# Kernel optimization log

Measured on AMD Instinct MI355X. Metric: run time of the kernel, lower is better.

## Reference

```python
import jax, jax.numpy as jnp
import numpy as np
import math

HEADS = 32
GROUPS = 8
HEAD_DIM = 64
HIDDEN = 2048
B, S = 2, 2048


def _rope(x, freqs_cis):
    # x: (..., S, head_dim); freqs_cis: (S, head_dim) -> interleaved cos/sin pattern
    x_even = x[..., ::2]
    x_odd = x[..., 1::2]
    cos = freqs_cis[..., ::2]
    sin = freqs_cis[..., 1::2]
    r_even = x_even * cos - x_odd * sin
    r_odd = x_even * sin + x_odd * cos
    return jnp.stack([r_even, r_odd], axis=-1).reshape(x.shape)


def setup_inputs() -> dict:
    key = jax.random.key(0)
    ks = jax.random.split(key, 12)
    scale = 1.0 / math.sqrt(HIDDEN)
    x = jax.random.normal(ks[0], (B, S, HIDDEN), dtype=jnp.float32)
    freqs_cis = jax.random.uniform(ks[1], (S, HEAD_DIM), dtype=jnp.float32)
    causal = jnp.tril(jnp.ones((S, S), dtype=bool))
    mask = jnp.where(causal, 0.0, -1e9).astype(jnp.float32)
    kv_dims = HEAD_DIM * GROUPS
    wq = jax.random.normal(ks[2], (HIDDEN, HIDDEN), jnp.float32) * scale
    bq = jnp.zeros((HIDDEN,), jnp.float32)
    wk = jax.random.normal(ks[3], (kv_dims, HIDDEN), jnp.float32) * scale
    bk = jnp.zeros((kv_dims,), jnp.float32)
    wv = jax.random.normal(ks[4], (kv_dims, HIDDEN), jnp.float32) * scale
    bv = jnp.zeros((kv_dims,), jnp.float32)
    wo = jax.random.normal(ks[5], (HIDDEN, HIDDEN), jnp.float32) * scale
    bo = jnp.zeros((HIDDEN,), jnp.float32)
    return dict(x=x, freqs_cis=freqs_cis, mask=mask, wq=wq, bq=bq,
                wk=wk, bk=bk, wv=wv, bv=bv, wo=wo, bo=bo)


def reference(x, freqs_cis, mask, wq, bq, wk, bk, wv, bv, wo, bo):
    b, s, h = x.shape
    rep = HEADS // GROUPS
    q = x @ wq.T + bq                      # (B,S,H)
    k = x @ wk.T + bk                      # (B,S,G*hd)
    v = x @ wv.T + bv
    q = q.reshape(b, s, HEADS, HEAD_DIM).transpose(0, 2, 1, 3)   # (B,Hh,S,hd)
    k = k.reshape(b, s, GROUPS, HEAD_DIM).transpose(0, 2, 1, 3)  # (B,G,S,hd)
    v = v.reshape(b, s, GROUPS, HEAD_DIM).transpose(0, 2, 1, 3)
    q = _rope(q, freqs_cis)
    k = _rope(k, freqs_cis)
    # GQA: group q heads instead of materially repeating K/V
    qg = q.reshape(b, GROUPS, rep, s, HEAD_DIM)
    scores = jnp.einsum('bgrsd,bgtd->bgrst', qg, k) / math.sqrt(HEAD_DIM)
    scores = scores + mask                 # broadcast (S,S)
    attn = jax.nn.softmax(scores, axis=-1)
    out = jnp.einsum('bgrst,bgtd->bgrsd', attn, v)
    out = out.reshape(b, HEADS, s, HEAD_DIM).transpose(0, 2, 1, 3).reshape(b, s, h)
    return out @ wo.T + bo
```

## Files before the change

### kernel.cpp

```cpp
#include <hip/hip_runtime.h>

#define S_LEN 2048
#define HID   2048
#define NQH   32
#define NKV   8
#define HD    64

#define BM 128
#define BN 128
#define BK 32

typedef __bf16 bf16x8 __attribute__((ext_vector_type(8)));
typedef __bf16 bf16x4 __attribute__((ext_vector_type(4)));
typedef float  f32x4  __attribute__((ext_vector_type(4)));

#define MFMA16(a, b, c) __builtin_amdgcn_mfma_f32_16x16x32_bf16(a, b, c, 0, 0, 0)

__device__ __forceinline__ void async_copy16(const void* g, void* l) {
  __builtin_amdgcn_global_load_lds(
      (const __attribute__((address_space(1))) unsigned int*)g,
      (__attribute__((address_space(3))) unsigned int*)l, 16, 0, 0);
}

__global__ void cast_all_k(const float* __restrict__ x,  const float* __restrict__ wq,
                           const float* __restrict__ wk, const float* __restrict__ wv,
                           const float* __restrict__ wo,
                           __bf16* __restrict__ xb,  __bf16* __restrict__ wqb,
                           __bf16* __restrict__ wkb, __bf16* __restrict__ wvb,
                           __bf16* __restrict__ wob) {
  int bid = blockIdx.x;
  const float* in; __bf16* out; int base;
  if (bid < 8192)       { in = x;  out = xb;  base = bid; }
  else if (bid < 12288) { in = wq; out = wqb; base = bid - 8192; }
  else if (bid < 13312) { in = wk; out = wkb; base = bid - 12288; }
  else if (bid < 14336) { in = wv; out = wvb; base = bid - 13312; }
  else                  { in = wo; out = wob; base = bid - 14336; }
  int i = (base * 256 + threadIdx.x) * 4;
  float4 v = *(const float4*)(in + i);
  bf16x4 o;
  o[0] = (__bf16)v.x; o[1] = (__bf16)v.y; o[2] = (__bf16)v.z; o[3] = (__bf16)v.w;
  *(bf16x4*)(out + i) = o;
}

__device__ __forceinline__ void gemm_pipe(const __bf16* __restrict__ A,
                                          const __bf16* __restrict__ B,
                                          int m0, int n0, int K,
                                          __bf16 (&As)[2][BM][BK],
                                          __bf16 (&Bs)[2][BN][BK],
                                          f32x4 (&acc)[4][4]) {
  const int tid = threadIdx.x, wave = tid >> 6, lane = tid & 63;
  const int l15 = lane & 15, quad = lane >> 4;
  const int wr = wave >> 1, wc = wave & 1;

  const int srow   = tid >> 2;
  const int schunk = (tid & 3) ^ ((tid >> 3) & 3);
  const __bf16* ga = A + (size_t)(m0 + srow) * K + schunk * 8;
  const __bf16* gb = B + (size_t)(n0 + srow) * K + schunk * 8;

  const int co = (quad ^ ((l15 >> 1) & 3)) * 8;

  const int NT = K / BK;

#define STAGE(st, kt) do {                                              \
    async_copy16(ga + (kt),                  &As[st][wave * 16][0]);    \
    async_copy16(ga + (kt) + (size_t)64 * K, &As[st][64 + wave * 16][0]); \
    async_copy16(gb + (kt),                  &Bs[st][wave * 16][0]);    \
    async_copy16(gb + (kt) + (size_t)64 * K, &Bs[st][64 + wave * 16][0]); \
  } while (0)

  STAGE(0, 0);
  asm volatile("s_waitcnt vmcnt(0)" ::: "memory");
  __builtin_amdgcn_s_barrier();
  asm volatile("" ::: "memory");

  int s = 0;
#pragma unroll 2
  for (int t = 0; t < NT; t++) {
    if (t + 1 < NT) STAGE(s ^ 1, (t + 1) * BK);

    const __bf16* a0 = &As[s][wr * 64][0];
    const __bf16* b0 = &Bs[s][wc * 64][0];
    bf16x8 af[4], bfr[4];
#pragma unroll
    for (int mt = 0; mt < 4; mt++)
      af[mt] = *(const bf16x8*)(a0 + (mt * 16 + l15) * BK + co);
#pragma unroll
    for (int nt = 0; nt < 4; nt++)
      bfr[nt] = *(const bf16x8*)(b0 + (nt * 16 + l15) * BK + co);

    __builtin_amdgcn_s_setprio(1);
#pragma unroll
    for (int mt = 0; mt < 4; mt++)
#pragma unroll
      for (int nt = 0; nt < 4; nt++)
        acc[mt][nt] = MFMA16(af[mt], bfr[nt], acc[mt][nt]);
    __builtin_amdgcn_s_setprio(0);

    asm volatile("s_waitcnt vmcnt(0) lgkmcnt(0)" ::: "memory");
    __builtin_amdgcn_s_barrier();
    asm volatile("" ::: "memory");
    s ^= 1;
  }
#undef STAGE
}

__global__ __launch_bounds__(256, 4) void gemm_qkv_k(const __bf16* __restrict__ xb,
    const __bf16* __restrict__ wqb, const __bf16* __restrict__ wkb, const __bf16* __restrict__ wvb,
    const float* __restrict__ bq, const float* __restrict__ bk, const float* __restrict__ bv,
    const float* __restrict__ fr,
    __bf16* __restrict__ Qb, __bf16* __restrict__ Kb, __bf16* __restrict__ Vt) {
  __shared__ __align__(16) __bf16 As[2][BM][BK];
  __shared__ __align__(16) __bf16 Bs[2][BN][BK];
  const int by = blockIdx.y;
  const int m0 = blockIdx.x * BM;
  const __bf16* B; const float* bias; int n0;
  int mode;
  if (by < 16)      { B = wqb; bias = bq; n0 = by * 128;        mode = 0; }
  else if (by < 20) { B = wkb; bias = bk; n0 = (by - 16) * 128; mode = 1; }
  else              { B = wvb; bias = bv; n0 = (by - 20) * 128; mode = 2; }

  f32x4 acc[4][4] = {};
  gemm_pipe(xb, B, m0, n0, HID, As, Bs, acc);

  const int tid = threadIdx.x, wave = tid >> 6, lane = tid & 63;
  const int l15 = lane & 15, quad = lane >> 4;
  const int wr = wave >> 1, wc = wave & 1;

  if (mode == 2) {
#pragma unroll
    for (int nt = 0; nt < 4; nt++) {
      int col = n0 + wc * 64 + nt * 16 + l15;
      int g = col >> 6, d = col & 63;
      float bv2 = bias[col];
#pragma unroll
      for (int mt = 0; mt < 4; mt++) {
        int row = m0 + wr * 64 + mt * 16 + quad * 4;
        int b = row >> 11, sI = row & 2047;
        bf16x4 o;
#pragma unroll
        for (int r = 0; r < 4; r++) o[r] = (__bf16)(acc[mt][nt][r] + bv2);
        *(bf16x4*)(Vt + (((size_t)(b * NKV + g) * HD + d)) * S_LEN + sI) = o;
      }
    }
  } else if (mode == 0) {
#pragma unroll
    for (int nt = 0; nt < 4; nt++) {
      int col = n0 + wc * 64 + nt * 16 + l15;
      float bv2 = bias[col];
#pragma unroll
      for (int mt = 0; mt < 4; mt++) {
        int row = m0 + wr * 64 + mt * 16 + quad * 4;
#pragma unroll
        for (int r = 0; r < 4; r++)
          Qb[(size_t)(row + r) * HID + col] = (__bf16)(acc[mt][nt][r] + bv2);
      }
    }
  } else {
    const int dpar = l15 & 1;
#pragma unroll
    for (int nt = 0; nt < 4; nt++) {
      int col = n0 + wc * 64 + nt * 16 + l15;
      int d = col & 63;
      float bv2 = bias[col];
#pragma unroll
      for (int mt = 0; mt < 4; mt++) {
        int row = m0 + wr * 64 + mt * 16 + quad * 4;
        int sI = row & 2047;
#pragma unroll
        for (int r = 0; r < 4; r++) {
          float v = acc[mt][nt][r] + bv2;
          float p = __shfl_xor(v, 1, 64);
          float f = fr[(size_t)(sI + r) * HD + d];
          float fp = __shfl_xor(f, 1, 64);
          float o = dpar ? (p * f + v * fp) : (v * f - p * fp);
          Kb[(size_t)(row + r) * 512 + col] = (__bf16)o;
        }
      }
    }
  }
}

__global__ __launch_bounds__(256, 4) void gemm_out_k(const __bf16* __restrict__ A,
    const __bf16* __restrict__ Bw, const float* __restrict__ bias, float* __restrict__ C) {
  __shared__ __align__(16) __bf16 As[2][BM][BK];
  __shared__ __align__(16) __bf16 Bs[2][BN][BK];
  const int m0 = blockIdx.x * BM, n0 = blockIdx.y * BN;
  f32x4 acc[4][4] = {};
  gemm_pipe(A, Bw, m0, n0, HID, As, Bs, acc);
  const int tid = threadIdx.x, wave = tid >> 6, lane = tid & 63;
  const int l15 = lane & 15, quad = lane >> 4;
  const int wr = wave >> 1, wc = wave & 1;
#pragma unroll
  for (int nt = 0; nt < 4; nt++) {
    int col = n0 + wc * 64 + nt * 16 + l15;
    float bv = bias[col];
#pragma unroll
    for (int mt = 0; mt < 4; mt++) {
      int row = m0 + wr * 64 + mt * 16 + quad * 4;
#pragma unroll
      for (int r = 0; r < 4; r++)
        C[(size_t)(row + r) * HID + col] = acc[mt][nt][r] + bv;
    }
  }
}

__device__ __forceinline__ void rope8(bf16x8& q, const float* f, float sc) {
  float4 fa = *(const float4*)f;
  float4 fb = *(const float4*)(f + 4);
  float e, o;
  e = (float)q[0]; o = (float)q[1];
  q[0] = (__bf16)((e * fa.x - o * fa.y) * sc);
  q[1] = (__bf16)((e * fa.y + o * fa.x) * sc);
  e = (float)q[2]; o = (float)q[3];
  q[2] = (__bf16)((e * fa.z - o * fa.w) * sc);
  q[3] = (__bf16)((e * fa.w + o * fa.z) * sc);
  e = (float)q[4]; o = (float)q[5];
  q[4] = (__bf16)((e * fb.x - o * fb.y) * sc);
  q[5] = (__bf16)((e * fb.y + o * fb.x) * sc);
  e = (float)q[6]; o = (float)q[7];
  q[6] = (__bf16)((e * fb.z - o * fb.w) * sc);
  q[7] = (__bf16)((e * fb.w + o * fb.z) * sc);
}

__global__ __launch_bounds__(256, 4) void flash_k(const __bf16* __restrict__ Q,
                                                  const __bf16* __restrict__ K,
                                                  const __bf16* __restrict__ Vt,
                                                  const float* __restrict__ fr,
                                                  __bf16* __restrict__ O) {
  __shared__ __align__(64) __bf16 Ksm[64][64];
  __shared__ __align__(64) __bf16 Vsm[64][64];
  __shared__ __align__(64) __bf16 Psm[4][16][64];
  const int tid = threadIdx.x;
  const int wave = tid >> 6, lane = tid & 63;
  const int l15 = lane & 15, quad = lane >> 4;
  const int x7 = l15 & 7, l15h = l15 >> 3;
  const int bh = blockIdx.x;
  const int b = bh >> 5, h = bh & 31, g = h >> 2;

  const int srow = tid >> 2, sc = (tid & 3) * 16;
  const int r7 = srow & 7;
  const int w0 = (((sc >> 3))     ^ r7) * 8;
  const int w1 = (((sc >> 3) + 1) ^ r7) * 8;

  char* kbp = (char*)&Ksm[0][0];
  char* vbp = (char*)&Vsm[0][0];
  char* pbp = (char*)&Psm[0][0][0];
  int kr[2], pr[2], pw[4];
#pragma unroll
  for (int ks = 0; ks < 2; ks++) {
    kr[ks] = l15 * 128 + (((ks * 4 + quad) ^ x7) * 16);
    pr[ks] = wave * 2048 + kr[ks];
  }
#pragma unroll
  for (int nt = 0; nt < 4; nt++)
    pw[nt] = wave * 2048 + quad * 512 + x7 * 2 + (((2 * nt + l15h) ^ ((quad & 1) * 4)) * 16);

  bf16x8 ones;
#pragma unroll
  for (int j = 0; j < 8; j++) ones[j] = (__bf16)1.0f;

  const __bf16* kbase = K + ((size_t)b * S_LEN + srow) * (NKV * HD) + g * HD + sc;
  const __bf16* vbase = Vt + (((size_t)b * NKV + g) * HD + srow) * S_LEN + sc;
  const float QSC = 0.125f * 1.44269504f;

#pragma unroll 1
  for (int half = 0; half < 2; half++) {
    const int qt = half ? (31 - (int)blockIdx.y) : (int)blockIdx.y;
    const int wq0 = qt * 64 + wave * 16;

    const __bf16* qp = Q + ((size_t)(b * S_LEN + wq0 + l15)) * HID + h * HD + quad * 8;
    bf16x8 qf0 = *(const bf16x8*)qp;
    bf16x8 qf1 = *(const bf16x8*)(qp + 32);
    const float* fq = fr + (size_t)(wq0 + l15) * HD + quad * 8;
    rope8(qf0, fq, QSC);
    rope8(qf1, fq + 32, QSC);

    f32x4 acc[4] = {};
    f32x4 accs = {};

    const __bf16* kp = kbase;
    const __bf16* vp = vbase;
    uint4 k0 = *(const uint4*)kp, k1 = *(const uint4*)(kp + 8);
    uint4 v0 = *(const uint4*)vp, v1 = *(const uint4*)(vp + 8);

    for (int t = 0; t <= qt; t++) {
      const int kv0 = t * 64;
      __syncthreads();
      *(uint4*)&Ksm[srow][w0] = k0;
      *(uint4*)&Ksm[srow][w1] = k1;
      *(uint4*)&Vsm[srow][w0] = v0;
      *(uint4*)&Vsm[srow][w1] = v1;
      if (t < qt) {
        kp += 64 * NKV * HD;  vp += 64;
        k0 = *(const uint4*)kp; k1 = *(const uint4*)(kp + 8);
        v0 = *(const uint4*)vp; v1 = *(const uint4*)(vp + 8);
      }
      __syncthreads();

      if (kv0 > wq0 + 15) continue;

      bf16x8 kf[2][4];
#pragma unroll
      for (int ks = 0; ks < 2; ks++)
#pragma unroll
        for (int nt = 0; nt < 4; nt++)
          kf[ks][nt] = *(const bf16x8*)(kbp + (kr[ks] + nt * 2048));

      f32x4 sacc[4] = {};
#pragma unroll
      for (int nt = 0; nt < 4; nt++) {
        sacc[nt] = MFMA16(qf0, kf[0][nt], sacc[nt]);
        sacc[nt] = MFMA16(qf1, kf[1][nt], sacc[nt]);
      }
      const bool domask = (kv0 + 63 > wq0);
#pragma unroll
      for (int nt = 0; nt < 4; nt++) {
        int kv = kv0 + nt * 16 + l15;
        int qr = wq0 + quad * 4;
#pragma unroll
        for (int r = 0; r < 4; r++) {
          float p = __builtin_exp2f(sacc[nt][r]);
          if (domask && kv > qr + r) p = 0.f;
          *(__bf16*)(pbp + ((pw[nt] ^ (r << 4)) + r * 128)) = (__bf16)p;
        }
      }

#pragma unroll
      for (int ks = 0; ks < 2; ks++) {
        bf16x8 vf[4];
#pragma unroll
        for (int nt = 0; nt < 4; nt++)
          vf[nt] = *(const bf16x8*)(vbp + (kr[ks] + nt * 2048));
        bf16x8 pf = *(const bf16x8*)(pbp + pr[ks]);
        accs = MFMA16(pf, ones, accs);
#pragma unroll
        for (int nt = 0; nt < 4; nt++)
          acc[nt] = MFMA16(pf, vf[nt], acc[nt]);
      }
    }

    __bf16* op = O + ((size_t)(b * S_LEN + wq0 + quad * 4)) * HID + h * HD;
    float inv[4];
#pragma unroll
    for (int r = 0; r < 4; r++) inv[r] = 1.f / accs[r];
#pragma unroll
    for (int nt = 0; nt < 4; nt++)
#pragma unroll
      for (int r = 0; r < 4; r++)
        op[(size_t)r * HID + nt * 16 + l15] = (__bf16)(acc[nt][r] * inv[r]);
  }
}

extern "C" void kernel_launch(void* const* d_in, const int* in_sizes, int n_in,
                              void* d_out, int out_size, void* d_ws, size_t ws_size,
                              hipStream_t stream) {
  (void)in_sizes; (void)n_in; (void)out_size; (void)ws_size;
  const float* x  = (const float*)d_in[0];
  const float* fr = (const float*)d_in[1];
  const float* wq = (const float*)d_in[3];
  const float* bq = (const float*)d_in[4];
  const float* wk = (const float*)d_in[5];
  const float* bk = (const float*)d_in[6];
  const float* wv = (const float*)d_in[7];
  const float* bv = (const float*)d_in[8];
  const float* wo = (const float*)d_in[9];
  const float* bo = (const float*)d_in[10];
  float* out = (float*)d_out;
  char* ws = (char*)d_ws;

  __bf16* xb  = (__bf16*)(ws);
  __bf16* wqb = (__bf16*)(ws + ((size_t)16 << 20));
  __bf16* wkb = (__bf16*)(ws + ((size_t)24 << 20));
  __bf16* wvb = (__bf16*)(ws + ((size_t)26 << 20));
  __bf16* wob = (__bf16*)(ws + ((size_t)28 << 20));
  __bf16* Qb  = (__bf16*)(ws + ((size_t)36 << 20));
  __bf16* Kb  = (__bf16*)(ws + ((size_t)52 << 20));
  __bf16* Vtb = (__bf16*)(ws + ((size_t)60 << 20));
  __bf16* Ab  = (__bf16*)(ws + ((size_t)64 << 20));

  cast_all_k<<<18432, 256, 0, stream>>>(x, wq, wk, wv, wo, xb, wqb, wkb, wvb, wob);

  gemm_qkv_k<<<dim3(32, 24), 256, 0, stream>>>(xb, wqb, wkb, wvb, bq, bk, bv, fr, Qb, Kb, Vtb);

  flash_k<<<dim3(64, 16), 256, 0, stream>>>(Qb, Kb, Vtb, fr, Ab);

  gemm_out_k<<<dim3(32, 16), 256, 0, stream>>>(Ab, wob, bo, out);
}
```

Measured before the change: 315.2 us.

## Keep P in registers via permlane swap and double-buffer K/V LDS tiles

The attention kernel no longer round-trips the probability tile through shared memory. It computes S transposed (K as the A operand) with a permuted K row order, packs the exp values to bf16 with v_cvt_pk_bf16_f32, and rearranges them across lanes with v_permlane32_swap so they feed the PV MFMA directly. K/V tiles are now double-buffered in LDS, which removes one of the two barriers per iteration and lets the next tile's store overlap compute. The cost is twice the K/V LDS footprint, which may affect occupancy, and a layout that depends on a subtle lane permutation.

```diff
diff --git a/kernel.cpp b/kernel.cpp
--- a/kernel.cpp
+++ b/kernel.cpp
@@ -20,6 +20,12 @@
   __builtin_amdgcn_global_load_lds(
       (const __attribute__((address_space(1))) unsigned int*)g,
       (__attribute__((address_space(3))) unsigned int*)l, 16, 0, 0);
+}
+
+__device__ __forceinline__ unsigned cvtpk_bf16(float lo, float hi) {
+  unsigned r;
+  asm("v_cvt_pk_bf16_f32 %0, %1, %2" : "=v"(r) : "v"(lo), "v"(hi));
+  return r;
 }
 
 __global__ void cast_all_k(const float* __restrict__ x,  const float* __restrict__ wq,
@@ -227,13 +233,11 @@
                                                   const __bf16* __restrict__ Vt,
                                                   const float* __restrict__ fr,
                                                   __bf16* __restrict__ O) {
-  __shared__ __align__(64) __bf16 Ksm[64][64];
-  __shared__ __align__(64) __bf16 Vsm[64][64];
-  __shared__ __align__(64) __bf16 Psm[4][16][64];
+  __shared__ __align__(64) __bf16 Ksm[2][64][64];
+  __shared__ __align__(64) __bf16 Vsm[2][64][64];
   const int tid = threadIdx.x;
   const int wave = tid >> 6, lane = tid & 63;
   const int l15 = lane & 15, quad = lane >> 4;
-  const int x7 = l15 & 7, l15h = l15 >> 3;
   const int bh = blockIdx.x;
   const int b = bh >> 5, h = bh & 31, g = h >> 2;
 
@@ -242,18 +246,19 @@
   const int w0 = (((sc >> 3))     ^ r7) * 8;
   const int w1 = (((sc >> 3) + 1) ^ r7) * 8;
 
-  char* kbp = (char*)&Ksm[0][0];
-  char* vbp = (char*)&Vsm[0][0];
-  char* pbp = (char*)&Psm[0][0][0];
-  int kr[2], pr[2], pw[4];
+  const char* kbp = (const char*)&Ksm[0][0][0];
+  const char* vbp = (const char*)&Vsm[0][0][0];
+
+  const int x7  = l15 & 7;
+  const int sig = 8 * ((l15 >> 2) & 1) + 4 * (l15 >> 3) + (l15 & 3);
+  const int s7  = sig & 7;
+  int krK[2], krV[2];
 #pragma unroll
   for (int ks = 0; ks < 2; ks++) {
-    kr[ks] = l15 * 128 + (((ks * 4 + quad) ^ x7) * 16);
-    pr[ks] = wave * 2048 + kr[ks];
+    krK[ks] = sig * 128 + (((ks * 4 + quad) ^ s7) * 16);
+    krV[ks] = l15 * 128 + (((ks * 4 + quad) ^ x7) * 16);
   }
-#pragma unroll
-  for (int nt = 0; nt < 4; nt++)
-    pw[nt] = wave * 2048 + quad * 512 + x7 * 2 + (((2 * nt + l15h) ^ ((quad & 1) * 4)) * 16);
+  const int kvb = 8 * (quad & 1) + 4 * (quad >> 1);
 
   bf16x8 ones;
 #pragma unroll
@@ -262,6 +267,7 @@
   const __bf16* kbase = K + ((size_t)b * S_LEN + srow) * (NKV * HD) + g * HD + sc;
   const __bf16* vbase = Vt + (((size_t)b * NKV + g) * HD + srow) * S_LEN + sc;
   const float QSC = 0.125f * 1.44269504f;
+  const int KSTEP = 64 * NKV * HD;
 
 #pragma unroll 1
   for (int half = 0; half < 2; half++) {
@@ -282,61 +288,89 @@
     const __bf16* vp = vbase;
     uint4 k0 = *(const uint4*)kp, k1 = *(const uint4*)(kp + 8);
     uint4 v0 = *(const uint4*)vp, v1 = *(const uint4*)(vp + 8);
-
+    *(uint4*)&Ksm[0][srow][w0] = k0;
+    *(uint4*)&Ksm[0][srow][w1] = k1;
+    *(uint4*)&Vsm[0][srow][w0] = v0;
+    *(uint4*)&Vsm[0][srow][w1] = v1;
+    if (qt > 0) {
+      kp += KSTEP;  vp += 64;
+      k0 = *(const uint4*)kp; k1 = *(const uint4*)(kp + 8);
+      v0 = *(const uint4*)vp; v1 = *(const uint4*)(vp + 8);
+    }
+    __syncthreads();
+
+#pragma unroll 1
     for (int t = 0; t <= qt; t++) {
+      const int cur = t & 1;
       const int kv0 = t * 64;
-      __syncthreads();
-      *(uint4*)&Ksm[srow][w0] = k0;
-      *(uint4*)&Ksm[srow][w1] = k1;
-      *(uint4*)&Vsm[srow][w0] = v0;
-      *(uint4*)&Vsm[srow][w1] = v1;
+
       if (t < qt) {
-        kp += 64 * NKV * HD;  vp += 64;
-        k0 = *(const uint4*)kp; k1 = *(const uint4*)(kp + 8);
-        v0 = *(const uint4*)vp; v1 = *(const uint4*)(vp + 8);
-      }
-      __syncthreads();
-
-      if (kv0 > wq0 + 15) continue;
-
-      bf16x8 kf[2][4];
-#pragma unroll
-      for (int ks = 0; ks < 2; ks++)
-#pragma unroll
-        for (int nt = 0; nt < 4; nt++)
-          kf[ks][nt] = *(const bf16x8*)(kbp + (kr[ks] + nt * 2048));
-
-      f32x4 sacc[4] = {};
-#pragma unroll
-      for (int nt = 0; nt < 4; nt++) {
-        sacc[nt] = MFMA16(qf0, kf[0][nt], sacc[nt]);
-        sacc[nt] = MFMA16(qf1, kf[1][nt], sacc[nt]);
-      }
-      const bool domask = (kv0 + 63 > wq0);
-#pragma unroll
-      for (int nt = 0; nt < 4; nt++) {
-        int kv = kv0 + nt * 16 + l15;
-        int qr = wq0 + quad * 4;
-#pragma unroll
-        for (int r = 0; r < 4; r++) {
-          float p = __builtin_exp2f(sacc[nt][r]);
-          if (domask && kv > qr + r) p = 0.f;
-          *(__bf16*)(pbp + ((pw[nt] ^ (r << 4)) + r * 128)) = (__bf16)p;
+        *(uint4*)&Ksm[cur ^ 1][srow][w0] = k0;
+        *(uint4*)&Ksm[cur ^ 1][srow][w1] = k1;
+        *(uint4*)&Vsm[cur ^ 1][srow][w0] = v0;
+        *(uint4*)&Vsm[cur ^ 1][srow][w1] = v1;
+        if (t + 2 <= qt) {
+          kp += KSTEP;  vp += 64;
+          k0 = *(const uint4*)kp; k1 = *(const uint4*)(kp + 8);
+          v0 = *(const uint4*)vp; v1 = *(const uint4*)(vp + 8);
         }
       }
 
-#pragma unroll
-      for (int ks = 0; ks < 2; ks++) {
-        bf16x8 vf[4];
-#pragma unroll
-        for (int nt = 0; nt < 4; nt++)
-          vf[nt] = *(const bf16x8*)(vbp + (kr[ks] + nt * 2048));
-        bf16x8 pf = *(const bf16x8*)(pbp + pr[ks]);
-        accs = MFMA16(pf, ones, accs);
-#pragma unroll
-        for (int nt = 0; nt < 4; nt++)
-          acc[nt] = MFMA16(pf, vf[nt], acc[nt]);
+      if (kv0 <= wq0 + 15) {
+        const int cb = cur * 8192;
+        bf16x8 kf[2][4];
+#pragma unroll
+        for (int ks = 0; ks < 2; ks++)
+#pragma unroll
+          for (int nt = 0; nt < 4; nt++)
+            kf[ks][nt] = *(const bf16x8*)(kbp + cb + krK[ks] + nt * 2048);
+
+        f32x4 sacc[4] = {};
+#pragma unroll
+        for (int nt = 0; nt < 4; nt++) {
+          sacc[nt] = MFMA16(kf[0][nt], qf0, sacc[nt]);
+          sacc[nt] = MFMA16(kf[1][nt], qf1, sacc[nt]);
+        }
+
+        const bool domask = (kv0 + 63 > wq0);
+        const int md = wq0 + l15 - kv0 - kvb;
+        unsigned W[4][2];
+#pragma unroll
+        for (int nt = 0; nt < 4; nt++) {
+          f32x4 pv;
+#pragma unroll
+          for (int r = 0; r < 4; r++) pv[r] = __builtin_exp2f(sacc[nt][r]);
+          if (domask) {
+#pragma unroll
+            for (int r = 0; r < 4; r++)
+              if (nt * 16 + r > md) pv[r] = 0.f;
+          }
+          W[nt][0] = cvtpk_bf16(pv[0], pv[1]);
+          W[nt][1] = cvtpk_bf16(pv[2], pv[3]);
+        }
+
+#pragma unroll
+        for (int ks = 0; ks < 2; ks++) {
+          unsigned a0 = W[2 * ks][0], b0 = W[2 * ks + 1][0];
+          unsigned a1 = W[2 * ks][1], b1 = W[2 * ks + 1][1];
+          asm("v_permlane32_swap_b32 %0, %1" : "+v"(a0), "+v"(b0));
+          asm("v_permlane32_swap_b32 %0, %1" : "+v"(a1), "+v"(b1));
+          union { unsigned u[4]; bf16x8 v; } pk;
+          pk.u[0] = a0; pk.u[1] = a1; pk.u[2] = b0; pk.u[3] = b1;
+          bf16x8 pf = pk.v;
+
+          bf16x8 vf[4];
+#pragma unroll
+          for (int nt = 0; nt < 4; nt++)
+            vf[nt] = *(const bf16x8*)(vbp + cb + krV[ks] + nt * 2048);
+          accs = MFMA16(pf, ones, accs);
+#pragma unroll
+          for (int nt = 0; nt < 4; nt++)
+            acc[nt] = MFMA16(pf, vf[nt], acc[nt]);
+        }
       }
+
+      __syncthreads();
     }
 
     __bf16* op = O + ((size_t)(b * S_LEN + wq0 + quad * 4)) * HID + h * HD;
```

Measured after the change: 309.6 us. No clear change (-1.8%).
